# Kernel tuning notes

Hardware: AMD Instinct MI355X
Metric: run time of the kernel (lower is better)

Reference implementation:

```python
import jax, jax.numpy as jnp
import numpy as np
from jax import lax

N, C1, C2, H, W = 4, 256, 256, 80, 80
CH = 128           # c_ = int(c2 * e)
G, KS = 1, 3       # groups, kernel_size
K = KS * KS        # sampling points per group
PAD, DIL = 1, 1
EPS_BN, EPS_LN = 1e-5, 1e-6


def conv_bn_silu(x, w, g, b, m, v, stride=1):
    # ultralytics Conv: conv(bias=False) + BatchNorm2d(eval) + SiLU
    pad = (w.shape[2] - 1) // 2
    y = lax.conv_general_dilated(x, w, (stride, stride), [(pad, pad), (pad, pad)],
                                 dimension_numbers=('NCHW', 'OIHW', 'NCHW'))
    s = g / jnp.sqrt(v + EPS_BN)
    y = y * s[None, :, None, None] + (b - m * s)[None, :, None, None]
    return jax.nn.silu(y)


def dcnv3_core(x, offset, mask):
    # x: (N,H,W,C) NHWC; offset: (N,H,W,G*K*2); mask: (N,H,W,G,K) softmaxed over K
    n, h, w, c = x.shape
    gc = c // G
    xp = jnp.pad(x, ((0, 0), (PAD, PAD), (PAD, PAD), (0, 0)))
    Hp, Wp = h + 2 * PAD, w + 2 * PAD
    base = (DIL * (KS - 1)) // 2
    # reference points (normalized by padded spatial size), stride 1
    ref_x = (jnp.arange(w, dtype=x.dtype) + base + 0.5) / Wp   # (W,)
    ref_y = (jnp.arange(h, dtype=x.dtype) + base + 0.5) / Hp   # (H,)
    gx = (jnp.arange(KS, dtype=x.dtype) * DIL - base) / Wp
    gy = (jnp.arange(KS, dtype=x.dtype) * DIL - base) / Hp
    grid_x = jnp.repeat(gx, KS)   # point p = i*KS + j -> x = gx[i]
    grid_y = jnp.tile(gy, KS)     # y = gy[j]  (torch meshgrid 'ij' ordering)
    off = offset.reshape(n, h, w, G, K, 2)
    loc_x = ref_x[None, None, :, None, None] + grid_x + off[..., 0] / Wp
    loc_y = ref_y[None, :, None, None, None] + grid_y + off[..., 1] / Hp
    # grid_sample align_corners=False: pixel = norm * size - 0.5
    px = loc_x * Wp - 0.5
    py = loc_y * Hp - 0.5
    x0 = jnp.floor(px); y0 = jnp.floor(py)
    lw, lh = px - x0, py - y0
    x0i, y0i = x0.astype(jnp.int32), y0.astype(jnp.int32)
    xv = jnp.transpose(xp.reshape(n, Hp * Wp, G, gc), (0, 2, 1, 3))  # (N,G,S,gc)
    tw = lambda a: jnp.transpose(a, (0, 3, 1, 2, 4))[..., None]      # (N,H,W,G,K)->(N,G,H,W,K,1)

    def gather(yi, xi):
        valid = ((xi >= 0) & (xi < Wp) & (yi >= 0) & (yi < Hp)).astype(x.dtype)
        idx = jnp.clip(yi, 0, Hp - 1) * Wp + jnp.clip(xi, 0, Wp - 1)
        idx = jnp.transpose(idx, (0, 3, 1, 2, 4)).reshape(n, G, h * w * K)
        v = jnp.take_along_axis(xv, idx[..., None], axis=2).reshape(n, G, h, w, K, gc)
        return v * tw(valid)   # zeros padding_mode

    out = (gather(y0i, x0i) * tw((1 - lh) * (1 - lw))
           + gather(y0i, x0i + 1) * tw((1 - lh) * lw)
           + gather(y0i + 1, x0i) * tw(lh * (1 - lw))
           + gather(y0i + 1, x0i + 1) * tw(lh * lw))   # (N,G,H,W,K,gc)
    m = jnp.transpose(mask, (0, 3, 1, 2, 4))[..., None]
    out = (out * m).sum(axis=4)                        # (N,G,H,W,gc)
    return jnp.transpose(out, (0, 2, 3, 1, 4)).reshape(n, h, w, c)


def forward(x, w1, g1, b1, m1, v1, w2, g2, b2, m2, v2,
            dw_w, dw_b, ln_g, ln_b, off_w, off_b, msk_w, msk_b,
            in_w, in_b, out_w, out_b, g3, b3, m3, v3):
    y = conv_bn_silu(x, w1, g1, b1, m1, v1)   # cv1: 3x3 Conv c1->c_
    y = conv_bn_silu(y, w2, g2, b2, m2, v2)   # cv2.conv: 1x1 Conv c_->c2
    t = jnp.transpose(y, (0, 2, 3, 1))        # NHWC
    x_proj = t @ in_w.T + in_b                # input_proj
    # dw_conv: depthwise 3x3 -> LayerNorm (channels_last) -> GELU
    dw = lax.conv_general_dilated(y, dw_w, (1, 1), [(1, 1), (1, 1)],
                                  dimension_numbers=('NCHW', 'OIHW', 'NCHW'),
                                  feature_group_count=C2)
    dw = jnp.transpose(dw, (0, 2, 3, 1)) + dw_b
    mu = dw.mean(-1, keepdims=True)
    var = ((dw - mu) ** 2).mean(-1, keepdims=True)
    dw = (dw - mu) / jnp.sqrt(var + EPS_LN) * ln_g + ln_b
    dw = jax.nn.gelu(dw, approximate=False)
    offset = dw @ off_w.T + off_b                                       # (N,H,W,G*K*2)
    mask = jax.nn.softmax((dw @ msk_w.T + msk_b).reshape(N, H, W, G, K), axis=-1)
    z = dcnv3_core(x_proj, offset, mask)
    z = z @ out_w.T + out_b                   # output_proj
    z = jnp.transpose(z, (0, 3, 1, 2))        # NCHW
    s = g3 / jnp.sqrt(v3 + EPS_BN)
    z = z * s[None, :, None, None] + (b3 - m3 * s)[None, :, None, None]
    z = jax.nn.silu(z)
    return x + z                              # shortcut (c1 == c2)


def setup_inputs():
    key = jax.random.key(0)
    ks = jax.random.split(key, 16)
    r = lambda k, s, sc=0.05: jax.random.normal(k, s, dtype=jnp.float32) * sc
    return {
        'x': jax.random.normal(ks[0], (N, C1, H, W), dtype=jnp.float32),
        'w1': r(ks[1], (CH, C1, 3, 3)),
        'g1': jnp.ones((CH,), jnp.float32), 'b1': jnp.zeros((CH,), jnp.float32),
        'm1': r(ks[2], (CH,), 0.1),
        'v1': jax.random.uniform(ks[3], (CH,), jnp.float32, 0.5, 1.5),
        'w2': r(ks[4], (C2, CH, 1, 1)),
        'g2': jnp.ones((C2,), jnp.float32), 'b2': jnp.zeros((C2,), jnp.float32),
        'm2': r(ks[5], (C2,), 0.1),
        'v2': jax.random.uniform(ks[6], (C2,), jnp.float32, 0.5, 1.5),
        'dw_w': r(ks[7], (C2, 1, 3, 3)), 'dw_b': jnp.zeros((C2,), jnp.float32),
        'ln_g': jnp.ones((C2,), jnp.float32), 'ln_b': jnp.zeros((C2,), jnp.float32),
        'off_w': r(ks[8], (G * K * 2, C2), 0.01), 'off_b': jnp.zeros((G * K * 2,), jnp.float32),
        'msk_w': r(ks[9], (G * K, C2), 0.01), 'msk_b': jnp.zeros((G * K,), jnp.float32),
        'in_w': r(ks[10], (C2, C2)), 'in_b': jnp.zeros((C2,), jnp.float32),
        'out_w': r(ks[11], (C2, C2)), 'out_b': jnp.zeros((C2,), jnp.float32),
        'g3': jnp.ones((C2,), jnp.float32), 'b3': jnp.zeros((C2,), jnp.float32),
        'm3': r(ks[12], (C2,), 0.1),
        'v3': jax.random.uniform(ks[13], (C2,), jnp.float32, 0.5, 1.5),
    }


def reference(x, w1, g1, b1, m1, v1, w2, g2, b2, m2, v2,
              dw_w, dw_b, ln_g, ln_b, off_w, off_b, msk_w, msk_b,
              in_w, in_b, out_w, out_b, g3, b3, m3, v3):
    return forward(x, w1, g1, b1, m1, v1, w2, g2, b2, m2, v2,
                   dw_w, dw_b, ln_g, ln_b, off_w, off_b, msk_w, msk_b,
                   in_w, in_b, out_w, out_b, g3, b3, m3, v3)
```

## Files before the change

### kernel.cpp

```cpp
#include <hip/hip_runtime.h>
#include <cmath>

#define TN 4
#define TC1 256
#define TCH 128
#define TC2 256
#define TH 80
#define TW 80
#define THP 82
#define TWP 84
#define NPIX (TN*TH*TW)

#define OFF_WBF   0
#define OFF_W2B   294912
#define OFF_INWB  327680
#define OFF_OUTWB 393216
#define OFF_DWT   458752
#define OFF_WCAT  461056
#define OFF_WCATB 467968
#define OFF_T1    468128
#define OFF_T2    468512
#define OFF_T3P   469024
#define OFF_XPAD  469504
#define OFF_Y1B   3997696
#define OFF_Y1P   7525888
#define OFF_Y2N   7525888
#define OFF_DWN   469504
#define OFF_RAWN  10802688
#define OFF_ZN    11493888

typedef __attribute__((ext_vector_type(8))) short bf16x8;
typedef __attribute__((ext_vector_type(4))) float f32x4;

__device__ __forceinline__ float siluf(float v) { return v / (1.f + expf(-v)); }
__device__ __forceinline__ short rnbf(float f) {
  unsigned u = __float_as_uint(f);
  unsigned r = (u + 0x7fffu + ((u >> 16) & 1u)) >> 16;
  return (short)r;
}
__device__ __forceinline__ float bf2f(short s) {
  return __uint_as_float(((unsigned)(unsigned short)s) << 16);
}

__global__ __launch_bounds__(256) void k_prep(
    const float* __restrict__ w1, const float* __restrict__ g1, const float* __restrict__ b1,
    const float* __restrict__ m1, const float* __restrict__ v1,
    const float* __restrict__ w2, const float* __restrict__ g2, const float* __restrict__ b2,
    const float* __restrict__ m2, const float* __restrict__ v2,
    const float* __restrict__ dww, const float* __restrict__ offw, const float* __restrict__ offb,
    const float* __restrict__ mskw, const float* __restrict__ mskb,
    const float* __restrict__ inw, const float* __restrict__ outw, const float* __restrict__ outb,
    const float* __restrict__ g3, const float* __restrict__ b3,
    const float* __restrict__ m3, const float* __restrict__ v3,
    float* __restrict__ ws)
{
  int i = blockIdx.x * 256 + threadIdx.x;
  if (i < 294912) {
    int co = i / 2304; int r = i - co * 2304;
    int tap = r >> 8; int ci = r & 255; int ky = tap / 3; int kx = tap - ky * 3;
    float s = g1[co] * __frsqrt_rn(v1[co] + 1e-5f);
    ((short*)(ws + OFF_WBF))[i] = rnbf(w1[((co * TC1 + ci) * 3 + ky) * 3 + kx] * s);
    return;
  }
  i -= 294912;
  if (i < 32768) {
    int co = i >> 7; int ci = i & 127;
    float s = g2[co] * __frsqrt_rn(v2[co] + 1e-5f);
    ((short*)(ws + OFF_W2B))[i] = rnbf(w2[co * TCH + ci] * s);
    return;
  }
  i -= 32768;
  if (i < 65536) {
    int co = i >> 8; int ci = i & 255;
    ((short*)(ws + OFF_INWB))[i] = rnbf(inw[co * TC2 + ci]);
    return;
  }
  i -= 65536;
  if (i < 65536) {
    int co = i >> 8; int ci = i & 255;
    float s = g3[co] * __frsqrt_rn(v3[co] + 1e-5f);
    ((short*)(ws + OFF_OUTWB))[i] = rnbf(outw[co * TC2 + ci] * s);
    return;
  }
  i -= 65536;
  if (i < 2304) { int c = i & 255; int j = i >> 8; ws[OFF_DWT + i] = dww[c * 9 + j]; return; }
  i -= 2304;
  if (i < 8192) {
    int c = i & 255; int j = i >> 8;
    float v = 0.f;
    if (j < 18) v = offw[j * 256 + c];
    else if (j < 27) v = mskw[(j - 18) * 256 + c];
    ((short*)(ws + OFF_WCAT))[i] = rnbf(v);
    return;
  }
  i -= 8192;
  if (i < 27) { ws[OFF_WCATB + i] = (i < 18) ? offb[i] : mskb[i - 18]; return; }
  i -= 27;
  if (i < 128) { float s = g1[i] / sqrtf(v1[i] + 1e-5f); ws[OFF_T1 + i] = b1[i] - m1[i] * s; return; }
  i -= 128;
  if (i < 256) { float s = g2[i] / sqrtf(v2[i] + 1e-5f); ws[OFF_T2 + i] = b2[i] - m2[i] * s; return; }
  i -= 256;
  if (i < 256) { float s = g3[i] / sqrtf(v3[i] + 1e-5f); ws[OFF_T3P + i] = outb[i] * s + b3[i] - m3[i] * s; return; }
}

__global__ __launch_bounds__(256) void k_padx(const float* __restrict__ x, short* __restrict__ xpn)
{
  __shared__ short lds[80 * 40];
  int b = blockIdx.x;
  int cc = b & 7; int hp = (b >> 3) % THP; int n = b / (THP * 8);
  int c0 = cc * 32;
  int t = threadIdx.x;
  int h = hp - 1;
  bool hv = (h >= 0 && h < TH);
  if (hv) {
    for (int f = t; f < 640; f += 256) {
      int ci = f / 20; int w4 = (f - ci * 20) * 4;
      float4 xv = *(const float4*)(x + ((n * TC1 + c0 + ci) * TH + h) * TW + w4);
      lds[(w4 + 0) * 40 + ci] = rnbf(xv.x);
      lds[(w4 + 1) * 40 + ci] = rnbf(xv.y);
      lds[(w4 + 2) * 40 + ci] = rnbf(xv.z);
      lds[(w4 + 3) * 40 + ci] = rnbf(xv.w);
    }
  }
  __syncthreads();
  short* op = xpn + ((n * THP + hp) * TWP) * TC2 + c0;
  for (int g = t; g < 672; g += 256) {
    int ci4 = (g & 7) * 4; int wp = g >> 3;
    short4 v = {0, 0, 0, 0};
    if (hv && wp >= 1 && wp <= TW) v = *(const short4*)(&lds[(wp - 1) * 40 + ci4]);
    *(short4*)(op + wp * TC2 + ci4) = v;
  }
}

#define A_STR 40
__global__ __launch_bounds__(256) void k_cv1(const short* __restrict__ xpn, const short* __restrict__ wbf,
                                             float* __restrict__ y1p)
{
  __shared__ short As[2][128 * A_STR];
  __shared__ short Bs[2][128 * A_STR];

  int b = blockIdx.x;
  int wt = b % 5; b /= 5; int ht = b % 10; b /= 10; int n = b & 3; int ks = b >> 2;
  int w0 = wt * 16, h0 = ht * 8;
  int tap0 = ks * 3;

  int tid = threadIdx.x;
  int wave = tid >> 6, lane = tid & 63;
  int ln = lane & 15, q = lane >> 4;
  int cohalf = (wave & 1) * 64;
  int pxhalf = (wave >> 1) * 64;

  int srow = tid >> 1;
  int ssub = (tid & 1) * 16;
  int hr = srow >> 4, wc = srow & 15;
  const short* arow = wbf + srow * 2304 + ssub;
  const short* brow = xpn + ((n * THP + h0 + hr) * TWP + (w0 + wc)) * 256 + ssub;

  f32x4 acc[4][4];
#pragma unroll
  for (int i = 0; i < 4; ++i)
#pragma unroll
    for (int j = 0; j < 4; ++j) acc[i][j] = (f32x4){0.f, 0.f, 0.f, 0.f};

  bf16x8 ra0, ra1, rb0, rb1;

  auto grab = [&](int c) {
    int rt = c >> 3;
    int atap = tap0 + rt;
    int ci0 = (c & 7) * 32;
    int ky = atap / 3, kx = atap - ky * 3;
    const short* ap = arow + atap * 256 + ci0;
    const short* bp = brow + (ky * TWP + kx) * 256 + ci0;
    ra0 = *(const bf16x8*)(ap);
    ra1 = *(const bf16x8*)(ap + 8);
    rb0 = *(const bf16x8*)(bp);
    rb1 = *(const bf16x8*)(bp + 8);
  };
  auto put = [&](int buf) {
    int o = srow * A_STR + ssub;
    *(bf16x8*)(&As[buf][o])     = ra0;
    *(bf16x8*)(&As[buf][o + 8]) = ra1;
    *(bf16x8*)(&Bs[buf][o])     = rb0;
    *(bf16x8*)(&Bs[buf][o + 8]) = rb1;
  };
  auto comp = [&](int buf) {
    bf16x8 af[4], bfv[4];
#pragma unroll
    for (int mt = 0; mt < 4; ++mt)
      af[mt] = *(const bf16x8*)(&As[buf][(cohalf + mt * 16 + ln) * A_STR + q * 8]);
#pragma unroll
    for (int nt = 0; nt < 4; ++nt)
      bfv[nt] = *(const bf16x8*)(&Bs[buf][(pxhalf + nt * 16 + ln) * A_STR + q * 8]);
#pragma unroll
    for (int mt = 0; mt < 4; ++mt)
#pragma unroll
      for (int nt = 0; nt < 4; ++nt)
        acc[mt][nt] = __builtin_amdgcn_mfma_f32_16x16x32_bf16(af[mt], bfv[nt], acc[mt][nt], 0, 0, 0);
  };

  grab(0);
  put(0);
  __syncthreads();
  for (int c = 0; c < 24; ++c) {
    if (c < 23) grab(c + 1);
    comp(c & 1);
    if (c < 23) {
      __syncthreads();
      put((c + 1) & 1);
      __syncthreads();
    }
  }

  float* yp = y1p + ks * (NPIX * TCH);
#pragma unroll
  for (int mt = 0; mt < 4; ++mt)
#pragma unroll
    for (int nt = 0; nt < 4; ++nt) {
      int p = pxhalf + nt * 16 + ln;
      int pr = p >> 4, pc = p & 15;
      int pix = (n * TH + h0 + pr) * TW + (w0 + pc);
      int co = cohalf + mt * 16 + q * 4;
      *(f32x4*)(yp + pix * TCH + co) = acc[mt][nt];
    }
}

__global__ __launch_bounds__(256) void k_y1red(const float* __restrict__ y1p, const float* __restrict__ t1v,
                                               short* __restrict__ y1b)
{
  int i = blockIdx.x * 256 + threadIdx.x;
  int co4 = (i & 31) * 4;
  int pix = i >> 5;
  float4 a = *(const float4*)(y1p + pix * TCH + co4);
  float4 bq = *(const float4*)(y1p + NPIX * TCH + pix * TCH + co4);
  float4 cq = *(const float4*)(y1p + 2 * NPIX * TCH + pix * TCH + co4);
  float4 t = *(const float4*)(t1v + co4);
  short4 o;
  o.x = rnbf(siluf(a.x + bq.x + cq.x + t.x));
  o.y = rnbf(siluf(a.y + bq.y + cq.y + t.y));
  o.z = rnbf(siluf(a.z + bq.z + cq.z + t.z));
  o.w = rnbf(siluf(a.w + bq.w + cq.w + t.w));
  *(short4*)(y1b + pix * TCH + co4) = o;
}

__global__ __launch_bounds__(256) void k_cv2(const short* __restrict__ y1b, const short* __restrict__ w2b,
                                             const float* __restrict__ t2v, short* __restrict__ y2b)
{
  __shared__ short As[2][128 * A_STR];
  __shared__ short Bs[2][128 * A_STR];

  int b = blockIdx.x;
  int ch = b & 1; int pt = b >> 1;
  int co_base = ch * 128;
  int pix0 = pt * 128;

  int tid = threadIdx.x;
  int wave = tid >> 6, lane = tid & 63;
  int ln = lane & 15, q = lane >> 4;
  int coh = (wave & 1) * 64;
  int pxh = (wave >> 1) * 64;

  int srow = tid >> 1;
  int ssub = (tid & 1) * 16;
  const short* arow = w2b + (co_base + srow) * TCH + ssub;
  const short* brow = y1b + (pix0 + srow) * TCH + ssub;

  f32x4 acc[4][4];
#pragma unroll
  for (int i = 0; i < 4; ++i)
#pragma unroll
    for (int j = 0; j < 4; ++j) acc[i][j] = (f32x4){0.f, 0.f, 0.f, 0.f};

  bf16x8 ra0, ra1, rb0, rb1;
  auto grab = [&](int c) {
    const short* ap = arow + c * 32;
    const short* bp = brow + c * 32;
    ra0 = *(const bf16x8*)(ap);
    ra1 = *(const bf16x8*)(ap + 8);
    rb0 = *(const bf16x8*)(bp);
    rb1 = *(const bf16x8*)(bp + 8);
  };
  auto put = [&](int buf) {
    int o = srow * A_STR + ssub;
    *(bf16x8*)(&As[buf][o])     = ra0;
    *(bf16x8*)(&As[buf][o + 8]) = ra1;
    *(bf16x8*)(&Bs[buf][o])     = rb0;
    *(bf16x8*)(&Bs[buf][o + 8]) = rb1;
  };
  auto comp = [&](int buf) {
    bf16x8 af[4], bfv[4];
#pragma unroll
    for (int mt = 0; mt < 4; ++mt)
      af[mt] = *(const bf16x8*)(&As[buf][(coh + mt * 16 + ln) * A_STR + q * 8]);
#pragma unroll
    for (int nt = 0; nt < 4; ++nt)
      bfv[nt] = *(const bf16x8*)(&Bs[buf][(pxh + nt * 16 + ln) * A_STR + q * 8]);
#pragma unroll
    for (int mt = 0; mt < 4; ++mt)
#pragma unroll
      for (int nt = 0; nt < 4; ++nt)
        acc[mt][nt] = __builtin_amdgcn_mfma_f32_16x16x32_bf16(af[mt], bfv[nt], acc[mt][nt], 0, 0, 0);
  };

  const int NCH = TCH / 32;
  grab(0);
  put(0);
  __syncthreads();
  for (int c = 0; c < NCH; ++c) {
    if (c < NCH - 1) grab(c + 1);
    comp(c & 1);
    if (c < NCH - 1) {
      __syncthreads();
      put((c + 1) & 1);
      __syncthreads();
    }
  }

#pragma unroll
  for (int mt = 0; mt < 4; ++mt) {
    int co = co_base + coh + mt * 16 + q * 4;
    float t0 = t2v[co], t1 = t2v[co + 1], t2 = t2v[co + 2], t3 = t2v[co + 3];
#pragma unroll
    for (int nt = 0; nt < 4; ++nt) {
      int pix = pix0 + pxh + nt * 16 + ln;
      short4 p;
      p.x = rnbf(siluf(acc[mt][nt][0] + t0));
      p.y = rnbf(siluf(acc[mt][nt][1] + t1));
      p.z = rnbf(siluf(acc[mt][nt][2] + t2));
      p.w = rnbf(siluf(acc[mt][nt][3] + t3));
      *(short4*)(y2b + pix * TC2 + co) = p;
    }
  }
}

__global__ __launch_bounds__(256) void k_proj_in(const short* __restrict__ y2b, const short* __restrict__ inwb,
                                                 const float* __restrict__ inb, short* __restrict__ xproj)
{
  __shared__ short As[2][128 * A_STR];
  __shared__ short Bs[2][128 * A_STR];

  int b = blockIdx.x;
  int ch = b & 1; int pt = b >> 1;
  int co_base = ch * 128;
  int pix0 = pt * 128;

  int tid = threadIdx.x;
  int wave = tid >> 6, lane = tid & 63;
  int ln = lane & 15, q = lane >> 4;
  int coh = (wave & 1) * 64;
  int pxh = (wave >> 1) * 64;

  int srow = tid >> 1;
  int ssub = (tid & 1) * 16;
  const short* arow = inwb + (co_base + srow) * TC2 + ssub;
  const short* brow = y2b + (pix0 + srow) * TC2 + ssub;

  f32x4 acc[4][4];
#pragma unroll
  for (int i = 0; i < 4; ++i)
#pragma unroll
    for (int j = 0; j < 4; ++j) acc[i][j] = (f32x4){0.f, 0.f, 0.f, 0.f};

  bf16x8 ra0, ra1, rb0, rb1;
  auto grab = [&](int c) {
    const short* ap = arow + c * 32;
    const short* bp = brow + c * 32;
    ra0 = *(const bf16x8*)(ap);
    ra1 = *(const bf16x8*)(ap + 8);
    rb0 = *(const bf16x8*)(bp);
    rb1 = *(const bf16x8*)(bp + 8);
  };
  auto put = [&](int buf) {
    int o = srow * A_STR + ssub;
    *(bf16x8*)(&As[buf][o])     = ra0;
    *(bf16x8*)(&As[buf][o + 8]) = ra1;
    *(bf16x8*)(&Bs[buf][o])     = rb0;
    *(bf16x8*)(&Bs[buf][o + 8]) = rb1;
  };
  auto comp = [&](int buf) {
    bf16x8 af[4], bfv[4];
#pragma unroll
    for (int mt = 0; mt < 4; ++mt)
      af[mt] = *(const bf16x8*)(&As[buf][(coh + mt * 16 + ln) * A_STR + q * 8]);
#pragma unroll
    for (int nt = 0; nt < 4; ++nt)
      bfv[nt] = *(const bf16x8*)(&Bs[buf][(pxh + nt * 16 + ln) * A_STR + q * 8]);
#pragma unroll
    for (int mt = 0; mt < 4; ++mt)
#pragma unroll
      for (int nt = 0; nt < 4; ++nt)
        acc[mt][nt] = __builtin_amdgcn_mfma_f32_16x16x32_bf16(af[mt], bfv[nt], acc[mt][nt], 0, 0, 0);
  };

  const int NCH = TC2 / 32;
  grab(0);
  put(0);
  __syncthreads();
  for (int c = 0; c < NCH; ++c) {
    if (c < NCH - 1) grab(c + 1);
    comp(c & 1);
    if (c < NCH - 1) {
      __syncthreads();
      put((c + 1) & 1);
      __syncthreads();
    }
  }

#pragma unroll
  for (int mt = 0; mt < 4; ++mt) {
    int co = co_base + coh + mt * 16 + q * 4;
    float b0 = inb[co], b1 = inb[co + 1], b2 = inb[co + 2], b3 = inb[co + 3];
#pragma unroll
    for (int nt = 0; nt < 4; ++nt) {
      int pix = pix0 + pxh + nt * 16 + ln;
      short4 p;
      p.x = rnbf(acc[mt][nt][0] + b0);
      p.y = rnbf(acc[mt][nt][1] + b1);
      p.z = rnbf(acc[mt][nt][2] + b2);
      p.w = rnbf(acc[mt][nt][3] + b3);
      *(short4*)(xproj + pix * TC2 + co) = p;
    }
  }
}

__global__ __launch_bounds__(256) void k_dwln(const short* __restrict__ y2b, const float* __restrict__ dwt,
                                              const float* __restrict__ dwb, const float* __restrict__ lng,
                                              const float* __restrict__ lnb, short* __restrict__ dwo)
{
  int tid = threadIdx.x;
  int wave = tid >> 6, lane = tid & 63;
  int half = lane >> 5;
  int pix = blockIdx.x * 8 + wave * 2 + half;
  int w = pix % TW; int h = (pix / TW) % TH; int n = pix / (TH * TW);
  int c0 = (lane & 31) * 8;

  float v[8];
  {
    float4 b0 = *(const float4*)(dwb + c0);
    float4 b1 = *(const float4*)(dwb + c0 + 4);
    v[0] = b0.x; v[1] = b0.y; v[2] = b0.z; v[3] = b0.w;
    v[4] = b1.x; v[5] = b1.y; v[6] = b1.z; v[7] = b1.w;
  }
#pragma unroll
  for (int dy = 0; dy < 3; ++dy) {
#pragma unroll
    for (int dx = 0; dx < 3; ++dx) {
      int hh = h + dy - 1, ww = w + dx - 1;
      bool ok = (hh >= 0) & (hh < TH) & (ww >= 0) & (ww < TW);
      int off = ok ? (((n * TH + hh) * TW + ww) * TC2 + c0) : c0;
      bf16x8 yv = *(const bf16x8*)(y2b + off);
      float m = ok ? 1.f : 0.f;
      const float* wp = dwt + (dy * 3 + dx) * TC2 + c0;
      float4 w0 = *(const float4*)(wp);
      float4 w1 = *(const float4*)(wp + 4);
      v[0] += bf2f(yv[0]) * w0.x * m;
      v[1] += bf2f(yv[1]) * w0.y * m;
      v[2] += bf2f(yv[2]) * w0.z * m;
      v[3] += bf2f(yv[3]) * w0.w * m;
      v[4] += bf2f(yv[4]) * w1.x * m;
      v[5] += bf2f(yv[5]) * w1.y * m;
      v[6] += bf2f(yv[6]) * w1.z * m;
      v[7] += bf2f(yv[7]) * w1.w * m;
    }
  }
  float sv = 0.f, sq = 0.f;
#pragma unroll
  for (int i = 0; i < 8; ++i) { sv += v[i]; sq += v[i] * v[i]; }
#pragma unroll
  for (int o = 16; o > 0; o >>= 1) { sv += __shfl_xor(sv, o); sq += __shfl_xor(sq, o); }
  float mu = sv * (1.f / 256.f);
  float var = sq * (1.f / 256.f) - mu * mu;
  float rs = 1.f / sqrtf(var + 1e-6f);
  float4 g0 = *(const float4*)(lng + c0);
  float4 g1 = *(const float4*)(lng + c0 + 4);
  float4 bb0 = *(const float4*)(lnb + c0);
  float4 bb1 = *(const float4*)(lnb + c0 + 4);
  float gv[8] = {g0.x, g0.y, g0.z, g0.w, g1.x, g1.y, g1.z, g1.w};
  float bv[8] = {bb0.x, bb0.y, bb0.z, bb0.w, bb1.x, bb1.y, bb1.z, bb1.w};
  const float is2 = 0.70710678118654752f;
  bf16x8 o8;
#pragma unroll
  for (int i = 0; i < 8; ++i) {
    float nv = (v[i] - mu) * rs * gv[i] + bv[i];
    o8[i] = rnbf(0.5f * nv * (1.f + erff(nv * is2)));
  }
  *(bf16x8*)(dwo + pix * TC2 + c0) = o8;
}

__global__ __launch_bounds__(256) void k_offmask(const short* __restrict__ dwo, const short* __restrict__ wcatb16,
                                                 const float* __restrict__ wcatb, float* __restrict__ raw)
{
  int tid = threadIdx.x;
  int wave = tid >> 6, lane = tid & 63;
  int ln = lane & 15, q = lane >> 4;
  int pix0 = blockIdx.x * 64 + wave * 16;

  f32x4 acc0 = {0.f, 0.f, 0.f, 0.f};
  f32x4 acc1 = acc0;

  const short* a0p = wcatb16 + ln * 256 + q * 8;
  const short* a1p = wcatb16 + (16 + ln) * 256 + q * 8;
  const short* bp  = dwo + (pix0 + ln) * 256 + q * 8;
#pragma unroll
  for (int kk = 0; kk < 256; kk += 32) {
    bf16x8 bf = *(const bf16x8*)(bp + kk);
    bf16x8 a0 = *(const bf16x8*)(a0p + kk);
    bf16x8 a1 = *(const bf16x8*)(a1p + kk);
    acc0 = __builtin_amdgcn_mfma_f32_16x16x32_bf16(a0, bf, acc0, 0, 0, 0);
    acc1 = __builtin_amdgcn_mfma_f32_16x16x32_bf16(a1, bf, acc1, 0, 0, 0);
  }

  int pix = pix0 + ln;
#pragma unroll
  for (int r = 0; r < 4; ++r) {
    int j0 = q * 4 + r;
    raw[pix * 27 + j0] = acc0[r] + wcatb[j0];
    int j1 = 16 + j0;
    if (j1 < 27) raw[pix * 27 + j1] = acc1[r] + wcatb[j1];
  }
}

__global__ __launch_bounds__(256) void k_dcn(const short* __restrict__ xproj, const float* __restrict__ raw,
                                             short* __restrict__ z)
{
  __shared__ int2 sp[8][36];
  int tid = threadIdx.x;
  int pixbase = blockIdx.x * 8;

  for (int j = tid; j < 288; j += 256) {
    int pxl = j / 36, t = j - pxl * 36;
    int pix = pixbase + pxl;
    int w = pix % TW; int h = (pix / TW) % TH;
    const float* r = raw + pix * 27;
    int k = t >> 2, tap = t & 3;
    int tx = tap & 1, ty = tap >> 1;
    float mx = r[18];
#pragma unroll
    for (int kk = 1; kk < 9; ++kk) mx = fmaxf(mx, r[18 + kk]);
    float sum = 0.f, ek = 0.f;
#pragma unroll
    for (int kk = 0; kk < 9; ++kk) {
      float ee = expf(r[18 + kk] - mx);
      sum += ee;
      if (kk == k) ek = ee;
    }
    float mk = ek / sum;
    float px = (float)(w + k / 3) + r[2 * k];
    float py = (float)(h + k % 3) + r[2 * k + 1];
    float x0f = floorf(px), y0f = floorf(py);
    float lw = px - x0f, lh = py - y0f;
    int x0 = (int)x0f + tx, y0 = (int)y0f + ty;
    float wt = mk * (tx ? lw : 1.f - lw) * (ty ? lh : 1.f - lh);
    bool valid = (x0 >= 1) & (x0 <= TW) & (y0 >= 1) & (y0 <= TH);
    int2 pr;
    pr.x = valid ? (((y0 - 1) * TW + (x0 - 1)) * TC2) : 0;
    pr.y = valid ? __float_as_int(wt) : 0;
    sp[pxl][t] = pr;
  }
  __syncthreads();

  int wave = tid >> 6, lane = tid & 63;
  int half = lane >> 5;
  int pxl = wave * 2 + half;
  int pix = pixbase + pxl;
  int n = pix / (TH * TW);
  int c0 = (lane & 31) * 8;
  const short* xb = xproj + n * (TH * TW * TC2) + c0;

  float a[8] = {0.f, 0.f, 0.f, 0.f, 0.f, 0.f, 0.f, 0.f};
#pragma unroll
  for (int t = 0; t < 36; ++t) {
    int2 pr = sp[pxl][t];
    float wt = __int_as_float(pr.y);
    bf16x8 v = *(const bf16x8*)(xb + pr.x);
#pragma unroll
    for (int i = 0; i < 8; ++i) a[i] += wt * bf2f(v[i]);
  }
  bf16x8 o8;
#pragma unroll
  for (int i = 0; i < 8; ++i) o8[i] = rnbf(a[i]);
  *(bf16x8*)(z + pix * TC2 + c0) = o8;
}

__global__ __launch_bounds__(256) void k_proj_out(const short* __restrict__ zb, const short* __restrict__ outwb,
                                                  const float* __restrict__ t3p,
                                                  const float* __restrict__ x, float* __restrict__ out)
{
  __shared__ short As[2][128 * A_STR];
  __shared__ short Bs[2][128 * A_STR];

  int b = blockIdx.x;
  int ch = b & 1; int pt = b >> 1;
  int co_base = ch * 128;
  int pix0 = pt * 128;

  int tid = threadIdx.x;
  int wave = tid >> 6, lane = tid & 63;
  int ln = lane & 15, q = lane >> 4;
  int coh = (wave & 1) * 64;
  int pxh = (wave >> 1) * 64;

  int srow = tid >> 1;
  int ssub = (tid & 1) * 16;
  const short* arow = outwb + (co_base + srow) * TC2 + ssub;
  const short* brow = zb + (pix0 + srow) * TC2 + ssub;

  f32x4 acc[4][4];
#pragma unroll
  for (int i = 0; i < 4; ++i)
#pragma unroll
    for (int j = 0; j < 4; ++j) acc[i][j] = (f32x4){0.f, 0.f, 0.f, 0.f};

  bf16x8 ra0, ra1, rb0, rb1;
  auto grab = [&](int c) {
    const short* ap = arow + c * 32;
    const short* bp = brow + c * 32;
    ra0 = *(const bf16x8*)(ap);
    ra1 = *(const bf16x8*)(ap + 8);
    rb0 = *(const bf16x8*)(bp);
    rb1 = *(const bf16x8*)(bp + 8);
  };
  auto put = [&](int buf) {
    int o = srow * A_STR + ssub;
    *(bf16x8*)(&As[buf][o])     = ra0;
    *(bf16x8*)(&As[buf][o + 8]) = ra1;
    *(bf16x8*)(&Bs[buf][o])     = rb0;
    *(bf16x8*)(&Bs[buf][o + 8]) = rb1;
  };
  auto comp = [&](int buf) {
    bf16x8 af[4], bfv[4];
#pragma unroll
    for (int mt = 0; mt < 4; ++mt)
      af[mt] = *(const bf16x8*)(&As[buf][(coh + mt * 16 + ln) * A_STR + q * 8]);
#pragma unroll
    for (int nt = 0; nt < 4; ++nt)
      bfv[nt] = *(const bf16x8*)(&Bs[buf][(pxh + nt * 16 + ln) * A_STR + q * 8]);
#pragma unroll
    for (int mt = 0; mt < 4; ++mt)
#pragma unroll
      for (int nt = 0; nt < 4; ++nt)
        acc[mt][nt] = __builtin_amdgcn_mfma_f32_16x16x32_bf16(af[mt], bfv[nt], acc[mt][nt], 0, 0, 0);
  };

  const int NCH = TC2 / 32;
  grab(0);
  put(0);
  __syncthreads();
  for (int c = 0; c < NCH; ++c) {
    if (c < NCH - 1) grab(c + 1);
    comp(c & 1);
    if (c < NCH - 1) {
      __syncthreads();
      put((c + 1) & 1);
      __syncthreads();
    }
  }

#pragma unroll
  for (int mt = 0; mt < 4; ++mt) {
    int co = co_base + coh + mt * 16 + q * 4;
#pragma unroll
    for (int nt = 0; nt < 4; ++nt) {
      int pix = pix0 + pxh + nt * 16 + ln;
      int n = pix / (TH * TW);
      int hw = pix - n * (TH * TW);
#pragma unroll
      for (int r = 0; r < 4; ++r) {
        int addr = (n * TC2 + co + r) * (TH * TW) + hw;
        out[addr] = x[addr] + siluf(acc[mt][nt][r] + t3p[co + r]);
      }
    }
  }
}

extern "C" void kernel_launch(void* const* d_in, const int* in_sizes, int n_in,
                              void* d_out, int out_size, void* d_ws, size_t ws_size,
                              hipStream_t stream)
{
  const float* x    = (const float*)d_in[0];
  const float* w1   = (const float*)d_in[1];
  const float* g1   = (const float*)d_in[2];
  const float* b1   = (const float*)d_in[3];
  const float* m1   = (const float*)d_in[4];
  const float* v1   = (const float*)d_in[5];
  const float* w2   = (const float*)d_in[6];
  const float* g2   = (const float*)d_in[7];
  const float* b2   = (const float*)d_in[8];
  const float* m2   = (const float*)d_in[9];
  const float* v2   = (const float*)d_in[10];
  const float* dww  = (const float*)d_in[11];
  const float* dwb  = (const float*)d_in[12];
  const float* lng  = (const float*)d_in[13];
  const float* lnb  = (const float*)d_in[14];
  const float* offw = (const float*)d_in[15];
  const float* offb = (const float*)d_in[16];
  const float* mskw = (const float*)d_in[17];
  const float* mskb = (const float*)d_in[18];
  const float* inw  = (const float*)d_in[19];
  const float* inb  = (const float*)d_in[20];
  const float* outw = (const float*)d_in[21];
  const float* outb = (const float*)d_in[22];
  const float* g3   = (const float*)d_in[23];
  const float* b3   = (const float*)d_in[24];
  const float* m3   = (const float*)d_in[25];
  const float* v3   = (const float*)d_in[26];

  float* ws  = (float*)d_ws;
  float* out = (float*)d_out;

  short* xpn    = (short*)(ws + OFF_XPAD);
  short* wbf    = (short*)(ws + OFF_WBF);
  short* w2b    = (short*)(ws + OFF_W2B);
  short* inwb   = (short*)(ws + OFF_INWB);
  short* outwb  = (short*)(ws + OFF_OUTWB);
  short* wcat16 = (short*)(ws + OFF_WCAT);
  float* y1p    = ws + OFF_Y1P;
  short* y1b    = (short*)(ws + OFF_Y1B);
  short* y2b    = (short*)(ws + OFF_Y2N);
  short* dwo    = (short*)(ws + OFF_DWN);
  float* raw    = ws + OFF_RAWN;
  short* zb     = (short*)(ws + OFF_ZN);
  short* xproj  = (short*)d_out;

  hipLaunchKernelGGL(k_prep, dim3(1836), dim3(256), 0, stream,
                     w1, g1, b1, m1, v1, w2, g2, b2, m2, v2,
                     dww, offw, offb, mskw, mskb, inw, outw, outb, g3, b3, m3, v3, ws);
  hipLaunchKernelGGL(k_padx,     dim3(TN * THP * 8), dim3(256), 0, stream, x, xpn);
  hipLaunchKernelGGL(k_cv1,      dim3(600),   dim3(256), 0, stream, xpn, wbf, y1p);
  hipLaunchKernelGGL(k_y1red,    dim3(3200),  dim3(256), 0, stream, y1p, ws + OFF_T1, y1b);
  hipLaunchKernelGGL(k_cv2,      dim3(400),   dim3(256), 0, stream, y1b, w2b, ws + OFF_T2, y2b);
  hipLaunchKernelGGL(k_proj_in,  dim3(400),   dim3(256), 0, stream, y2b, inwb, inb, xproj);
  hipLaunchKernelGGL(k_dwln,     dim3(3200),  dim3(256), 0, stream, y2b, ws + OFF_DWT, dwb, lng, lnb, dwo);
  hipLaunchKernelGGL(k_offmask,  dim3(400),   dim3(256), 0, stream, dwo, wcat16, ws + OFF_WCATB, raw);
  hipLaunchKernelGGL(k_dcn,      dim3(3200),  dim3(256), 0, stream, xproj, raw, zb);
  hipLaunchKernelGGL(k_proj_out, dim3(400),   dim3(256), 0, stream, zb, outwb, ws + OFF_T3P, x, out);
}
```

Measured before the change: 273.3 us.

## Stage GEMM tiles with direct global-to-LDS loads and XOR-swizzled layout

```diff
diff --git a/kernel.cpp b/kernel.cpp
--- a/kernel.cpp
+++ b/kernel.cpp
@@ -42,6 +42,12 @@
   return __uint_as_float(((unsigned)(unsigned short)s) << 16);
 }
 
+typedef __attribute__((address_space(1))) const unsigned int guint_t;
+typedef __attribute__((address_space(3))) unsigned int luint_t;
+__device__ __forceinline__ void gl2lds16(const short* g, short* l) {
+  __builtin_amdgcn_global_load_lds((guint_t*)g, (luint_t*)l, 16, 0, 0);
+}
+
 __global__ __launch_bounds__(256) void k_prep(
     const float* __restrict__ w1, const float* __restrict__ g1, const float* __restrict__ b1,
     const float* __restrict__ m1, const float* __restrict__ v1,
@@ -132,12 +138,11 @@
   }
 }
 
-#define A_STR 40
 __global__ __launch_bounds__(256) void k_cv1(const short* __restrict__ xpn, const short* __restrict__ wbf,
                                              float* __restrict__ y1p)
 {
-  __shared__ short As[2][128 * A_STR];
-  __shared__ short Bs[2][128 * A_STR];
+  __shared__ short As[2][4096] __attribute__((aligned(16)));
+  __shared__ short Bs[2][4096] __attribute__((aligned(16)));
 
   int b = blockIdx.x;
   int wt = b % 5; b /= 5; int ht = b % 10; b /= 10; int n = b & 3; int ks = b >> 2;
@@ -150,11 +155,8 @@
   int cohalf = (wave & 1) * 64;
   int pxhalf = (wave >> 1) * 64;
 
-  int srow = tid >> 1;
-  int ssub = (tid & 1) * 16;
-  int hr = srow >> 4, wc = srow & 15;
-  const short* arow = wbf + srow * 2304 + ssub;
-  const short* brow = xpn + ((n * THP + h0 + hr) * TWP + (w0 + wc)) * 256 + ssub;
+  int lr = lane & 15;
+  int lp = ((lane >> 4) ^ (lane & 3)) * 8;
 
   f32x4 acc[4][4];
 #pragma unroll
@@ -162,35 +164,33 @@
 #pragma unroll
     for (int j = 0; j < 4; ++j) acc[i][j] = (f32x4){0.f, 0.f, 0.f, 0.f};
 
-  bf16x8 ra0, ra1, rb0, rb1;
-
-  auto grab = [&](int c) {
+  auto stage = [&](int c, int buf) {
     int rt = c >> 3;
     int atap = tap0 + rt;
     int ci0 = (c & 7) * 32;
     int ky = atap / 3, kx = atap - ky * 3;
-    const short* ap = arow + atap * 256 + ci0;
-    const short* bp = brow + (ky * TWP + kx) * 256 + ci0;
-    ra0 = *(const bf16x8*)(ap);
-    ra1 = *(const bf16x8*)(ap + 8);
-    rb0 = *(const bf16x8*)(bp);
-    rb1 = *(const bf16x8*)(bp + 8);
-  };
-  auto put = [&](int buf) {
-    int o = srow * A_STR + ssub;
-    *(bf16x8*)(&As[buf][o])     = ra0;
-    *(bf16x8*)(&As[buf][o + 8]) = ra1;
-    *(bf16x8*)(&Bs[buf][o])     = rb0;
-    *(bf16x8*)(&Bs[buf][o + 8]) = rb1;
+#pragma unroll
+    for (int i = 0; i < 4; ++i) {
+      int seg = wave * 4 + i;
+      if (seg < 8) {
+        const short* g = wbf + (seg * 16 + lr) * 2304 + atap * 256 + ci0 + lp;
+        gl2lds16(g, &As[buf][seg * 512]);
+      } else {
+        int s = seg - 8;
+        const short* g = xpn + (((n * THP + h0 + s + ky) * TWP) + (w0 + lr + kx)) * 256 + ci0 + lp;
+        gl2lds16(g, &Bs[buf][s * 512]);
+      }
+    }
   };
   auto comp = [&](int buf) {
+    int xo = ((q ^ (ln & 3)) * 16 + ln) * 8;
     bf16x8 af[4], bfv[4];
 #pragma unroll
     for (int mt = 0; mt < 4; ++mt)
-      af[mt] = *(const bf16x8*)(&As[buf][(cohalf + mt * 16 + ln) * A_STR + q * 8]);
+      af[mt] = *(const bf16x8*)(&As[buf][((cohalf >> 4) + mt) * 512 + xo]);
 #pragma unroll
     for (int nt = 0; nt < 4; ++nt)
-      bfv[nt] = *(const bf16x8*)(&Bs[buf][(pxhalf + nt * 16 + ln) * A_STR + q * 8]);
+      bfv[nt] = *(const bf16x8*)(&Bs[buf][((pxhalf >> 4) + nt) * 512 + xo]);
 #pragma unroll
     for (int mt = 0; mt < 4; ++mt)
 #pragma unroll
@@ -198,17 +198,12 @@
         acc[mt][nt] = __builtin_amdgcn_mfma_f32_16x16x32_bf16(af[mt], bfv[nt], acc[mt][nt], 0, 0, 0);
   };
 
-  grab(0);
-  put(0);
+  stage(0, 0);
   __syncthreads();
   for (int c = 0; c < 24; ++c) {
-    if (c < 23) grab(c + 1);
+    if (c < 23) stage(c + 1, (c + 1) & 1);
     comp(c & 1);
-    if (c < 23) {
-      __syncthreads();
-      put((c + 1) & 1);
-      __syncthreads();
-    }
+    if (c < 23) __syncthreads();
   }
 
   float* yp = y1p + ks * (NPIX * TCH);
@@ -245,8 +240,8 @@
 __global__ __launch_bounds__(256) void k_cv2(const short* __restrict__ y1b, const short* __restrict__ w2b,
                                              const float* __restrict__ t2v, short* __restrict__ y2b)
 {
-  __shared__ short As[2][128 * A_STR];
-  __shared__ short Bs[2][128 * A_STR];
+  __shared__ short As[2][4096] __attribute__((aligned(16)));
+  __shared__ short Bs[2][4096] __attribute__((aligned(16)));
 
   int b = blockIdx.x;
   int ch = b & 1; int pt = b >> 1;
@@ -259,10 +254,8 @@
   int coh = (wave & 1) * 64;
   int pxh = (wave >> 1) * 64;
 
-  int srow = tid >> 1;
-  int ssub = (tid & 1) * 16;
-  const short* arow = w2b + (co_base + srow) * TCH + ssub;
-  const short* brow = y1b + (pix0 + srow) * TCH + ssub;
+  int lr = lane & 15;
+  int lp = ((lane >> 4) ^ (lane & 3)) * 8;
 
   f32x4 acc[4][4];
 #pragma unroll
@@ -270,30 +263,29 @@
 #pragma unroll
     for (int j = 0; j < 4; ++j) acc[i][j] = (f32x4){0.f, 0.f, 0.f, 0.f};
 
-  bf16x8 ra0, ra1, rb0, rb1;
-  auto grab = [&](int c) {
-    const short* ap = arow + c * 32;
-    const short* bp = brow + c * 32;
-    ra0 = *(const bf16x8*)(ap);
-    ra1 = *(const bf16x8*)(ap + 8);
-    rb0 = *(const bf16x8*)(bp);
-    rb1 = *(const bf16x8*)(bp + 8);
-  };
-  auto put = [&](int buf) {
-    int o = srow * A_STR + ssub;
-    *(bf16x8*)(&As[buf][o])     = ra0;
-    *(bf16x8*)(&As[buf][o + 8]) = ra1;
-    *(bf16x8*)(&Bs[buf][o])     = rb0;
-    *(bf16x8*)(&Bs[buf][o + 8]) = rb1;
+  auto stage = [&](int c, int buf) {
+#pragma unroll
+    for (int i = 0; i < 4; ++i) {
+      int seg = wave * 4 + i;
+      if (seg < 8) {
+        const short* g = w2b + (co_base + seg * 16 + lr) * TCH + c * 32 + lp;
+        gl2lds16(g, &As[buf][seg * 512]);
+      } else {
+        int s = seg - 8;
+        const short* g = y1b + (pix0 + s * 16 + lr) * TCH + c * 32 + lp;
+        gl2lds16(g, &Bs[buf][s * 512]);
+      }
+    }
   };
   auto comp = [&](int buf) {
+    int xo = ((q ^ (ln & 3)) * 16 + ln) * 8;
     bf16x8 af[4], bfv[4];
 #pragma unroll
     for (int mt = 0; mt < 4; ++mt)
-      af[mt] = *(const bf16x8*)(&As[buf][(coh + mt * 16 + ln) * A_STR + q * 8]);
+      af[mt] = *(const bf16x8*)(&As[buf][((coh >> 4) + mt) * 512 + xo]);
 #pragma unroll
     for (int nt = 0; nt < 4; ++nt)
-      bfv[nt] = *(const bf16x8*)(&Bs[buf][(pxh + nt * 16 + ln) * A_STR + q * 8]);
+      bfv[nt] = *(const bf16x8*)(&Bs[buf][((pxh >> 4) + nt) * 512 + xo]);
 #pragma unroll
     for (int mt = 0; mt < 4; ++mt)
 #pragma unroll
@@ -302,17 +294,12 @@
   };
 
   const int NCH = TCH / 32;
-  grab(0);
-  put(0);
+  stage(0, 0);
   __syncthreads();
   for (int c = 0; c < NCH; ++c) {
-    if (c < NCH - 1) grab(c + 1);
+    if (c < NCH - 1) stage(c + 1, (c + 1) & 1);
     comp(c & 1);
-    if (c < NCH - 1) {
-      __syncthreads();
-      put((c + 1) & 1);
-      __syncthreads();
-    }
+    if (c < NCH - 1) __syncthreads();
   }
 
 #pragma unroll
@@ -335,8 +322,8 @@
 __global__ __launch_bounds__(256) void k_proj_in(const short* __restrict__ y2b, const short* __restrict__ inwb,
                                                  const float* __restrict__ inb, short* __restrict__ xproj)
 {
-  __shared__ short As[2][128 * A_STR];
-  __shared__ short Bs[2][128 * A_STR];
+  __shared__ short As[2][4096] __attribute__((aligned(16)));
+  __shared__ short Bs[2][4096] __attribute__((aligned(16)));
 
   int b = blockIdx.x;
   int ch = b & 1; int pt = b >> 1;
@@ -349,10 +336,8 @@
   int coh = (wave & 1) * 64;
   int pxh = (wave >> 1) * 64;
 
-  int srow = tid >> 1;
-  int ssub = (tid & 1) * 16;
-  const short* arow = inwb + (co_base + srow) * TC2 + ssub;
-  const short* brow = y2b + (pix0 + srow) * TC2 + ssub;
+  int lr = lane & 15;
+  int lp = ((lane >> 4) ^ (lane & 3)) * 8;
 
   f32x4 acc[4][4];
 #pragma unroll
@@ -360,30 +345,29 @@
 #pragma unroll
     for (int j = 0; j < 4; ++j) acc[i][j] = (f32x4){0.f, 0.f, 0.f, 0.f};
 
-  bf16x8 ra0, ra1, rb0, rb1;
-  auto grab = [&](int c) {
-    const short* ap = arow + c * 32;
-    const short* bp = brow + c * 32;
-    ra0 = *(const bf16x8*)(ap);
-    ra1 = *(const bf16x8*)(ap + 8);
-    rb0 = *(const bf16x8*)(bp);
-    rb1 = *(const bf16x8*)(bp + 8);
-  };
-  auto put = [&](int buf) {
-    int o = srow * A_STR + ssub;
-    *(bf16x8*)(&As[buf][o])     = ra0;
-    *(bf16x8*)(&As[buf][o + 8]) = ra1;
-    *(bf16x8*)(&Bs[buf][o])     = rb0;
-    *(bf16x8*)(&Bs[buf][o + 8]) = rb1;
+  auto stage = [&](int c, int buf) {
+#pragma unroll
+    for (int i = 0; i < 4; ++i) {
+      int seg = wave * 4 + i;
+      if (seg < 8) {
+        const short* g = inwb + (co_base + seg * 16 + lr) * TC2 + c * 32 + lp;
+        gl2lds16(g, &As[buf][seg * 512]);
+      } else {
+        int s = seg - 8;
+        const short* g = y2b + (pix0 + s * 16 + lr) * TC2 + c * 32 + lp;
+        gl2lds16(g, &Bs[buf][s * 512]);
+      }
+    }
   };
   auto comp = [&](int buf) {
+    int xo = ((q ^ (ln & 3)) * 16 + ln) * 8;
     bf16x8 af[4], bfv[4];
 #pragma unroll
     for (int mt = 0; mt < 4; ++mt)
-      af[mt] = *(const bf16x8*)(&As[buf][(coh + mt * 16 + ln) * A_STR + q * 8]);
+      af[mt] = *(const bf16x8*)(&As[buf][((coh >> 4) + mt) * 512 + xo]);
 #pragma unroll
     for (int nt = 0; nt < 4; ++nt)
-      bfv[nt] = *(const bf16x8*)(&Bs[buf][(pxh + nt * 16 + ln) * A_STR + q * 8]);
+      bfv[nt] = *(const bf16x8*)(&Bs[buf][((pxh >> 4) + nt) * 512 + xo]);
 #pragma unroll
     for (int mt = 0; mt < 4; ++mt)
 #pragma unroll
@@ -392,17 +376,12 @@
   };
 
   const int NCH = TC2 / 32;
-  grab(0);
-  put(0);
+  stage(0, 0);
   __syncthreads();
   for (int c = 0; c < NCH; ++c) {
-    if (c < NCH - 1) grab(c + 1);
+    if (c < NCH - 1) stage(c + 1, (c + 1) & 1);
     comp(c & 1);
-    if (c < NCH - 1) {
-      __syncthreads();
-      put((c + 1) & 1);
-      __syncthreads();
-    }
+    if (c < NCH - 1) __syncthreads();
   }
 
 #pragma unroll
@@ -585,8 +564,8 @@
                                                   const float* __restrict__ t3p,
                                                   const float* __restrict__ x, float* __restrict__ out)
 {
-  __shared__ short As[2][128 * A_STR];
-  __shared__ short Bs[2][128 * A_STR];
+  __shared__ short As[2][4096] __attribute__((aligned(16)));
+  __shared__ short Bs[2][4096] __attribute__((aligned(16)));
 
   int b = blockIdx.x;
   int ch = b & 1; int pt = b >> 1;
@@ -599,10 +578,8 @@
   int coh = (wave & 1) * 64;
   int pxh = (wave >> 1) * 64;
 
-  int srow = tid >> 1;
-  int ssub = (tid & 1) * 16;
-  const short* arow = outwb + (co_base + srow) * TC2 + ssub;
-  const short* brow = zb + (pix0 + srow) * TC2 + ssub;
+  int lr = lane & 15;
+  int lp = ((lane >> 4) ^ (lane & 3)) * 8;
 
   f32x4 acc[4][4];
 #pragma unroll
@@ -610,30 +587,29 @@
 #pragma unroll
     for (int j = 0; j < 4; ++j) acc[i][j] = (f32x4){0.f, 0.f, 0.f, 0.f};
 
-  bf16x8 ra0, ra1, rb0, rb1;
-  auto grab = [&](int c) {
-    const short* ap = arow + c * 32;
-    const short* bp = brow + c * 32;
-    ra0 = *(const bf16x8*)(ap);
-    ra1 = *(const bf16x8*)(ap + 8);
-    rb0 = *(const bf16x8*)(bp);
-    rb1 = *(const bf16x8*)(bp + 8);
-  };
-  auto put = [&](int buf) {
-    int o = srow * A_STR + ssub;
-    *(bf16x8*)(&As[buf][o])     = ra0;
-    *(bf16x8*)(&As[buf][o + 8]) = ra1;
-    *(bf16x8*)(&Bs[buf][o])     = rb0;
-    *(bf16x8*)(&Bs[buf][o + 8]) = rb1;
+  auto stage = [&](int c, int buf) {
+#pragma unroll
+    for (int i = 0; i < 4; ++i) {
+      int seg = wave * 4 + i;
+      if (seg < 8) {
+        const short* g = outwb + (co_base + seg * 16 + lr) * TC2 + c * 32 + lp;
+        gl2lds16(g, &As[buf][seg * 512]);
+      } else {
+        int s = seg - 8;
+        const short* g = zb + (pix0 + s * 16 + lr) * TC2 + c * 32 + lp;
+        gl2lds16(g, &Bs[buf][s * 512]);
+      }
+    }
   };
   auto comp = [&](int buf) {
+    int xo = ((q ^ (ln & 3)) * 16 + ln) * 8;
     bf16x8 af[4], bfv[4];
 #pragma unroll
     for (int mt = 0; mt < 4; ++mt)
-      af[mt] = *(const bf16x8*)(&As[buf][(coh + mt * 16 + ln) * A_STR + q * 8]);
+      af[mt] = *(const bf16x8*)(&As[buf][((coh >> 4) + mt) * 512 + xo]);
 #pragma unroll
     for (int nt = 0; nt < 4; ++nt)
-      bfv[nt] = *(const bf16x8*)(&Bs[buf][(pxh + nt * 16 + ln) * A_STR + q * 8]);
+      bfv[nt] = *(const bf16x8*)(&Bs[buf][((pxh >> 4) + nt) * 512 + xo]);
 #pragma unroll
     for (int mt = 0; mt < 4; ++mt)
 #pragma unroll
@@ -642,17 +618,12 @@
   };
 
   const int NCH = TC2 / 32;
-  grab(0);
-  put(0);
+  stage(0, 0);
   __syncthreads();
   for (int c = 0; c < NCH; ++c) {
-    if (c < NCH - 1) grab(c + 1);
+    if (c < NCH - 1) stage(c + 1, (c + 1) & 1);
     comp(c & 1);
-    if (c < NCH - 1) {
-      __syncthreads();
-      put((c + 1) & 1);
-      __syncthreads();
-    }
+    if (c < NCH - 1) __syncthreads();
   }
 
 #pragma unroll
```

Result: no change. 274.2 us (+0.3%).
